# Optimization experiments

Measured on AMD Instinct MI355X. Metric: run time of the kernel, lower is better.

The kernel has to match this reference:

```python
import jax, jax.numpy as jnp
import numpy as np

DILATED = (1, 2, 3)
NUM_PROTOS = 100
PROTO_SIZE = 4
ENC_SIZE = 1600
NUM_CLASSES = 2
B, L = 64, 256

# num_filters split exactly as in torch: floor(P/len) each, first gets remainder
_nf = [NUM_PROTOS // len(DILATED)] * len(DILATED)
_nf[0] += NUM_PROTOS % len(DILATED)
NUM_FILTERS = tuple(_nf)  # (34, 33, 33)


def setup_inputs() -> dict:
    key = jax.random.key(0)
    k1, k2, k3 = jax.random.split(key, 3)
    embedding = jax.random.normal(k1, (B, L, ENC_SIZE), dtype=jnp.float32)
    # nn.init.uniform_ default is U[0,1)
    protolayer = jax.random.uniform(k2, (NUM_PROTOS, ENC_SIZE, PROTO_SIZE), dtype=jnp.float32)
    fc_w = jax.random.normal(k3, (NUM_CLASSES, NUM_PROTOS), dtype=jnp.float32) * 0.1
    return {"embedding": embedding, "protolayer": protolayer, "fc_w": fc_w}


def _l2_convolution(x_bel, protolayer):
    # x_bel: [B, L, E] -> [B, E, L] for NCH conv layout
    x = jnp.transpose(x_bel, (0, 2, 1))
    # sliding-window sum of x^2 computed ONCE per dilation (shared across protos,
    # mathematically identical to conv1d with all-ones weight)
    s = jnp.sum(x * x, axis=1)  # [B, L]
    p2_sum = jnp.sum(protolayer * protolayer, axis=(1, 2))  # [P]
    distances = []
    j = 0
    Lx = x.shape[2]
    for d, n in zip(DILATED, NUM_FILTERS):
        L_out = Lx - (PROTO_SIZE - 1) * d
        # windowed sum over K=PROTO_SIZE taps with dilation d: [B, L_out]
        x2_patch = sum(s[:, k * d:k * d + L_out] for k in range(PROTO_SIZE))
        # dilated cross-correlation x * p : [B, n, L_out]
        xp = jax.lax.conv_general_dilated(
            x, protolayer[j:j + n],
            window_strides=(1,), padding='VALID', rhs_dilation=(d,),
            dimension_numbers=('NCH', 'OIH', 'NCH'))
        dist = jnp.sqrt(jnp.abs(x2_patch[:, None, :] - 2.0 * xp
                                + p2_sum[j:j + n][None, :, None]))
        distances.append(dist)
        j += n
    return distances


def reference(embedding, protolayer, fc_w):
    distances = _l2_convolution(embedding, protolayer)
    prototype_distances = jnp.concatenate(
        [jnp.min(d, axis=2) for d in distances], axis=1)  # [B, P]
    class_out = prototype_distances @ fc_w.T  # [B, num_classes]
    return (prototype_distances, distances[0], distances[1], distances[2], class_out)
```

## Files before the change

kernel.cpp:

```cpp
#include <hip/hip_runtime.h>

#define B_   64
#define L_   256
#define E_   1600
#define P_   100
#define KP   4
#define N0 34
#define N1 33
#define N2 33
#define LOUT0 253
#define LOUT1 250
#define LOUT2 247
#define OFF_PD 0
#define OFF_D0 6400
#define OFF_D1 (OFF_D0 + B_*N0*LOUT0)
#define OFF_D2 (OFF_D1 + B_*N1*LOUT1)
#define OFF_CO (OFF_D2 + B_*N2*LOUT2)

#define WS_BT   0ull
#define WS_P2   1280000ull
#define WS_NEED (WS_P2 + 512ull)

#define TM2   144
#define BOFF4 36864

typedef float f32x4 __attribute__((ext_vector_type(4)));
typedef float f32x8 __attribute__((ext_vector_type(8)));
typedef unsigned short ushort8v __attribute__((ext_vector_type(8)));
typedef __bf16 bf16x8 __attribute__((ext_vector_type(8)));
typedef _Float16 f16;

__device__ __forceinline__ unsigned short bf16rne(float f) {
    unsigned u = __float_as_uint(f);
    u += 0x7FFFu + ((u >> 16) & 1u);
    return (unsigned short)(u >> 16);
}

typedef __attribute__((address_space(3))) void lds_void_t;
typedef __attribute__((address_space(1))) void glb_void_t;

__device__ __forceinline__ void gload16(const void* g, void* l) {
    __builtin_amdgcn_global_load_lds((const glb_void_t*)g, (lds_void_t*)l, 16, 0, 0);
}


__global__ __launch_bounds__(256) void proto_prepB_fast(
        const float* __restrict__ proto, char* __restrict__ ws,
        float* __restrict__ out) {
    int q = blockIdx.x;
    int wave = threadIdx.x >> 6, lane = threadIdx.x & 63;
    if (q < 25) {
        int p = q * 4 + wave;
        const float4* r = (const float4*)(proto + (size_t)p * (E_ * KP));
        unsigned short* bt = (unsigned short*)(ws + WS_BT);
        float acc = 0.f;
        #pragma unroll
        for (int it = 0; it < 25; ++it) {
            int e = it * 64 + lane;
            float4 v = r[e];
            acc += v.x*v.x + v.y*v.y + v.z*v.z + v.w*v.w;
            bt[(size_t)(4*p + 0) * E_ + e] = bf16rne(v.x);
            bt[(size_t)(4*p + 1) * E_ + e] = bf16rne(v.y);
            bt[(size_t)(4*p + 2) * E_ + e] = bf16rne(v.z);
            bt[(size_t)(4*p + 3) * E_ + e] = bf16rne(v.w);
        }
        #pragma unroll
        for (int off = 32; off; off >>= 1) acc += __shfl_down(acc, off);
        if (lane == 0) ((float*)(ws + WS_P2))[p] = acc;
    } else {
        for (int i = threadIdx.x; i < B_ * P_; i += 256)
            out[OFF_PD + i] = __uint_as_float(0x7F800000u);
    }
}

__global__ __launch_bounds__(192, 4) void proto_main_f32(
        const float* __restrict__ emb, const char* __restrict__ ws,
        float* __restrict__ out) {

    __shared__ __align__(16) char smem[47104];

    int bx    = blockIdx.x;
    int lb    = (bx & 7) * 80 + (bx >> 3);
    int b     = lb / 10;
    int inner = lb % 10;
    int m     = inner / 5;
    int n_blk = inner % 5;
    int r0    = m ? 112 : 0;
    int pbase = n_blk * 20;

    const char* Ag = (const char*)(emb + (size_t)(b * L_ + r0) * E_);
    const char* Bg = ws + WS_BT + (size_t)(pbase * 4) * 3200;

    int tid  = threadIdx.x;
    int lane = tid & 63;
    int wave = tid >> 6;
    int mrow = lane & 15;
    int jq   = lane >> 4;
    int a_lr = lane >> 4;
    int a_sl = lane & 15;
    int b_lr = lane >> 3;
    int b_sl = lane & 7;

    f32x4 acc[3][5] = {};
    float sacc[3] = {0.f, 0.f, 0.f};

    for (int c = 0; c < 25; ++c) {
        const char* Ac = Ag + c * 256;
        const char* Bc = Bg + c * 128;

        for (int t = wave; t < 10; t += 3) {
            int row = t * 8 + b_lr;
            gload16(Bc + (size_t)row * 3200 + ((b_sl ^ (row & 7)) * 16),
                    smem + BOFF4 + t * 1024);
        }
        for (int t = wave; t < 36; t += 3) {
            int row = t * 4 + a_lr;
            gload16(Ac + (size_t)row * 6400 + ((a_sl ^ (row & 15)) * 16),
                    smem + t * 1024);
        }
        __syncthreads();

        #pragma unroll
        for (int ks = 0; ks < 2; ++ks) {
            ushort8v af[3];
            #pragma unroll
            for (int mi = 0; mi < 3; ++mi) {
                int r  = wave * 48 + mi * 16 + mrow;
                int s0 = ks * 8 + jq * 2;
                f32x4 f0 = *(const f32x4*)(smem + r * 256 + ((s0 ^ (r & 15)) * 16));
                f32x4 f1 = *(const f32x4*)(smem + r * 256 + (((s0 + 1) ^ (r & 15)) * 16));
                sacc[mi] += f0[0]*f0[0] + f0[1]*f0[1] + f0[2]*f0[2] + f0[3]*f0[3]
                          + f1[0]*f1[0] + f1[1]*f1[1] + f1[2]*f1[2] + f1[3]*f1[3];
                f32x8 fv;
                fv[0]=f0[0]; fv[1]=f0[1]; fv[2]=f0[2]; fv[3]=f0[3];
                fv[4]=f1[0]; fv[5]=f1[1]; fv[6]=f1[2]; fv[7]=f1[3];
                af[mi] = __builtin_bit_cast(ushort8v,
                            __builtin_convertvector(fv, bf16x8));
            }
            ushort8v bfv[5];
            #pragma unroll
            for (int ni = 0; ni < 5; ++ni) {
                int rowB = ni * 16 + mrow;
                bfv[ni] = *(const ushort8v*)(smem + BOFF4 + rowB * 128
                            + (((ks << 2) + jq) ^ (rowB & 7)) * 16);
            }
            #pragma unroll
            for (int mi = 0; mi < 3; ++mi)
                #pragma unroll
                for (int ni = 0; ni < 5; ++ni)
                    acc[mi][ni] = __builtin_amdgcn_mfma_f32_16x16x32_bf16(
                        __builtin_bit_cast(bf16x8, af[mi]),
                        __builtin_bit_cast(bf16x8, bfv[ni]),
                        acc[mi][ni], 0, 0, 0);
        }
        __syncthreads();
    }

    f16*      Yh     = (f16*)smem;
    float*    slds   = (float*)(smem + 23328);
    float*    p2lds  = (float*)(smem + 23328 + 576);
    unsigned* minlds = (unsigned*)(smem + 23328 + 656);

    {
        int colq = lane & 15;
        int rowq = (lane >> 4) * 4;
        #pragma unroll
        for (int mi = 0; mi < 3; ++mi) {
            int row = wave * 48 + mi * 16 + rowq;
            #pragma unroll
            for (int ni = 0; ni < 5; ++ni) {
                int col = ni * 16 + colq;
                #pragma unroll
                for (int r = 0; r < 4; ++r)
                    Yh[(row + r) * 81 + col] = (f16)acc[mi][ni][r];
            }
        }
    }
    #pragma unroll
    for (int mi = 0; mi < 3; ++mi) {
        float v = sacc[mi];
        v += __shfl_xor(v, 16);
        v += __shfl_xor(v, 32);
        sacc[mi] = v;
    }
    if (jq == 0) {
        #pragma unroll
        for (int mi = 0; mi < 3; ++mi)
            slds[wave * 48 + mi * 16 + mrow] = sacc[mi];
    }
    if (tid < 20) {
        p2lds[tid] = ((const float*)(ws + WS_P2))[pbase + tid];
        minlds[tid] = 0x7F800000u;
    }
    __syncthreads();

    int l_lo = m * 128;
    for (int idx = tid; idx < 20 * 128; idx += 192) {
        int pl  = idx >> 7;
        int lof = idx & 127;
        int p = pbase + pl;
        int d, Lout, nseg, pseg; size_t segbase;
        if (p < 34)      { d = 1; Lout = LOUT0; segbase = OFF_D0; pseg = p;      nseg = N0; }
        else if (p < 67) { d = 2; Lout = LOUT1; segbase = OFF_D1; pseg = p - 34; nseg = N1; }
        else             { d = 3; Lout = LOUT2; segbase = OFF_D2; pseg = p - 67; nseg = N2; }
        int l = l_lo + lof;
        if (l < Lout) {
            int rl = l - r0;
            int c0 = pl * 4;
            float xp = (float)Yh[rl * 81 + c0]
                     + (float)Yh[(rl + d) * 81 + c0 + 1]
                     + (float)Yh[(rl + 2*d) * 81 + c0 + 2]
                     + (float)Yh[(rl + 3*d) * 81 + c0 + 3];
            float x2 = slds[rl] + slds[rl + d] + slds[rl + 2*d] + slds[rl + 3*d];
            float dist = sqrtf(fabsf(x2 - 2.f * xp + p2lds[pl]));
            out[segbase + ((size_t)b * nseg + pseg) * Lout + l] = dist;
            atomicMin(&minlds[pl], __float_as_uint(dist));
        }
    }
    __syncthreads();
    if (tid < 20)
        atomicMin((unsigned*)out + OFF_PD + b * P_ + pbase + tid, minlds[tid]);
}

#define TM   144
#define ASTR 40
#define YSTR 81

__global__ __launch_bounds__(256) void proto_prep_kernel(
        const float* __restrict__ emb, const float* __restrict__ proto,
        float* __restrict__ ws_s, float* __restrict__ ws_p2,
        float* __restrict__ out) {
    int q = blockIdx.x;
    int wave = threadIdx.x >> 6, lane = threadIdx.x & 63;
    if (q < 4096) {
        int row = q * 4 + wave;
        const float4* r = (const float4*)(emb + (size_t)row * E_);
        float acc = 0.f;
        #pragma unroll
        for (int it = 0; it < 7; ++it) {
            int e4 = it * 64 + lane;
            if (e4 < 400) {
                float4 v = r[e4];
                acc += v.x*v.x + v.y*v.y + v.z*v.z + v.w*v.w;
            }
        }
        #pragma unroll
        for (int off = 32; off; off >>= 1) acc += __shfl_down(acc, off);
        if (lane == 0) ws_s[row] = acc;
    } else if (q < 4121) {
        int p = (q - 4096) * 4 + wave;
        if (p < P_) {
            const float4* r = (const float4*)(proto + (size_t)p * (E_ * KP));
            float acc = 0.f;
            #pragma unroll
            for (int it = 0; it < 25; ++it) {
                float4 v = r[it * 64 + lane];
                acc += v.x*v.x + v.y*v.y + v.z*v.z + v.w*v.w;
            }
            #pragma unroll
            for (int off = 32; off; off >>= 1) acc += __shfl_down(acc, off);
            if (lane == 0) ws_p2[p] = acc;
        }
    } else {
        for (int i = threadIdx.x; i < B_ * P_; i += 256)
            out[OFF_PD + i] = __uint_as_float(0x7F800000u);
    }
}

__global__ __launch_bounds__(192) void proto_main_kernel(
        const float* __restrict__ emb, const float* __restrict__ proto,
        const float* __restrict__ ws_s, const float* __restrict__ ws_p2,
        float* __restrict__ out) {

    __shared__ __align__(16) char smem[47392];
    unsigned short* Ald = (unsigned short*)smem;
    unsigned short* Bld = (unsigned short*)(smem + TM*ASTR*2);

    int bx = blockIdx.x;
    int n_blk = bx % 5;
    int m     = (bx / 5) & 1;
    int b     = bx / 10;
    int r0    = m ? 112 : 0;
    int pbase = n_blk * 20;

    const float* Abase = emb + ((size_t)(b * L_ + r0)) * E_;
    const float* Bbase = proto + (size_t)pbase * (E_ * KP);

    int tid  = threadIdx.x;
    int lane = tid & 63;
    int wave = tid >> 6;
    int mrow = lane & 15;
    int kq   = (lane >> 4) * 8;

    f32x4 acc[3][5] = {};

    for (int c = 0; c < E_ / 32; ++c) {
        int e0 = c * 32;
        #pragma unroll
        for (int i = 0; i < 6; ++i) {
            int idx = tid + i * 192;
            int row = idx >> 3;
            int e4  = idx & 7;
            float4 v = *(const float4*)(Abase + (size_t)row * E_ + e0 + e4 * 4);
            ushort4 bv = make_ushort4(bf16rne(v.x), bf16rne(v.y),
                                      bf16rne(v.z), bf16rne(v.w));
            *(ushort4*)&Ald[row * ASTR + e4 * 4] = bv;
        }
        for (int idx = tid; idx < 640; idx += 192) {
            int pl = idx >> 5;
            int el = idx & 31;
            float4 v = *(const float4*)(Bbase + (size_t)pl * (E_ * KP)
                                        + (size_t)(e0 + el) * KP);
            Bld[(4*pl + 0) * ASTR + el] = bf16rne(v.x);
            Bld[(4*pl + 1) * ASTR + el] = bf16rne(v.y);
            Bld[(4*pl + 2) * ASTR + el] = bf16rne(v.z);
            Bld[(4*pl + 3) * ASTR + el] = bf16rne(v.w);
        }
        __syncthreads();

        ushort8v af[3], bfr[5];
        #pragma unroll
        for (int mi = 0; mi < 3; ++mi)
            af[mi] = *(const ushort8v*)&Ald[(wave*48 + mi*16 + mrow) * ASTR + kq];
        #pragma unroll
        for (int ni = 0; ni < 5; ++ni)
            bfr[ni] = *(const ushort8v*)&Bld[(ni*16 + mrow) * ASTR + kq];
        #pragma unroll
        for (int mi = 0; mi < 3; ++mi)
            #pragma unroll
            for (int ni = 0; ni < 5; ++ni)
                acc[mi][ni] = __builtin_amdgcn_mfma_f32_16x16x32_bf16(
                    __builtin_bit_cast(bf16x8, af[mi]),
                    __builtin_bit_cast(bf16x8, bfr[ni]),
                    acc[mi][ni], 0, 0, 0);
        __syncthreads();
    }

    float*    Ylds   = (float*)smem;
    float*    slds   = (float*)(smem + TM * YSTR * 4);
    float*    p2lds  = slds + TM;
    unsigned* minlds = (unsigned*)(p2lds + 20);

    {
        int colq = lane & 15;
        int rowq = (lane >> 4) * 4;
        #pragma unroll
        for (int mi = 0; mi < 3; ++mi) {
            int row = wave * 48 + mi * 16 + rowq;
            #pragma unroll
            for (int ni = 0; ni < 5; ++ni) {
                int col = ni * 16 + colq;
                #pragma unroll
                for (int r = 0; r < 4; ++r)
                    Ylds[(row + r) * YSTR + col] = acc[mi][ni][r];
            }
        }
    }
    if (tid < TM) slds[tid] = ws_s[b * L_ + r0 + tid];
    if (tid < 20) { p2lds[tid] = ws_p2[pbase + tid]; minlds[tid] = 0x7F800000u; }
    __syncthreads();

    int l_lo = m * 128;
    for (int idx = tid; idx < 20 * 128; idx += 192) {
        int pl  = idx >> 7;
        int lof = idx & 127;
        int p = pbase + pl;
        int d, Lout, nseg, pseg; size_t segbase;
        if (p < 34)      { d = 1; Lout = LOUT0; segbase = OFF_D0; pseg = p;      nseg = N0; }
        else if (p < 67) { d = 2; Lout = LOUT1; segbase = OFF_D1; pseg = p - 34; nseg = N1; }
        else             { d = 3; Lout = LOUT2; segbase = OFF_D2; pseg = p - 67; nseg = N2; }
        int l = l_lo + lof;
        if (l < Lout) {
            int rl = l - r0;
            int c0 = pl * 4;
            float xp = Ylds[rl * YSTR + c0]
                     + Ylds[(rl + d) * YSTR + c0 + 1]
                     + Ylds[(rl + 2*d) * YSTR + c0 + 2]
                     + Ylds[(rl + 3*d) * YSTR + c0 + 3];
            float x2 = slds[rl] + slds[rl + d] + slds[rl + 2*d] + slds[rl + 3*d];
            float dist = sqrtf(fabsf(x2 - 2.f * xp + p2lds[pl]));
            out[segbase + ((size_t)b * nseg + pseg) * Lout + l] = dist;
            atomicMin(&minlds[pl], __float_as_uint(dist));
        }
    }
    __syncthreads();
    if (tid < 20)
        atomicMin((unsigned*)out + OFF_PD + b * P_ + pbase + tid, minlds[tid]);
}

__global__ __launch_bounds__(128) void proto_fc_kernel(
        const float* __restrict__ fc_w, float* __restrict__ out) {
    int t = threadIdx.x;
    int b = t >> 1, c = t & 1;
    const float* pd = out + OFF_PD + b * P_;
    const float* w  = fc_w + c * P_;
    float s = 0.f;
    #pragma unroll 4
    for (int p = 0; p < P_; ++p) s += pd[p] * w[p];
    out[OFF_CO + b * 2 + c] = s;
}

extern "C" void kernel_launch(void* const* d_in, const int* in_sizes, int n_in,
                              void* d_out, int out_size, void* d_ws, size_t ws_size,
                              hipStream_t stream) {
    const float* emb   = (const float*)d_in[0];
    const float* proto = (const float*)d_in[1];
    const float* fc_w  = (const float*)d_in[2];
    float* out  = (float*)d_out;

    if (ws_size >= WS_NEED) {
        char* ws = (char*)d_ws;
        proto_prepB_fast<<<26, 256, 0, stream>>>(proto, ws, out);
        proto_main_f32<<<640, 192, 0, stream>>>(emb, ws, out);
    } else {
        float* ws_s  = (float*)d_ws;
        float* ws_p2 = ws_s + B_ * L_;
        proto_prep_kernel<<<4122, 256, 0, stream>>>(emb, proto, ws_s, ws_p2, out);
        proto_main_kernel<<<640, 192, 0, stream>>>(emb, proto, ws_s, ws_p2, out);
    }
    proto_fc_kernel<<<1, 128, 0, stream>>>(fc_w, out);
}
```

Baseline: 215.8 us.

## Load GEMM operands directly from global into registers, pre-permute B fragments

The main GEMM loop no longer stages A (embedding) and B (bf16 prototypes) tiles through LDS with global_load_lds and barriers. Each lane now reads its MFMA fragments straight from global memory. The prep kernel writes the prototype matrix in a fragment-permuted layout, so each lane's B read is one contiguous 16-byte load. This removes LDS staging traffic and the per-chunk __syncthreads, and shrinks LDS use. In exchange, the A loads are strided 32-byte reads per lane with no software pipelining, the occupancy hint drops from 4 to 2, and latency hiding relies on having many waves in flight.

```diff
diff --git a/kernel.cpp b/kernel.cpp
--- a/kernel.cpp
+++ b/kernel.cpp
@@ -18,11 +18,8 @@
 #define OFF_CO (OFF_D2 + B_*N2*LOUT2)
 
 #define WS_BT   0ull
-#define WS_P2   1280000ull
+#define WS_P2   1310720ull
 #define WS_NEED (WS_P2 + 512ull)
-
-#define TM2   144
-#define BOFF4 36864
 
 typedef float f32x4 __attribute__((ext_vector_type(4)));
 typedef float f32x8 __attribute__((ext_vector_type(8)));
@@ -36,15 +33,8 @@
     return (unsigned short)(u >> 16);
 }
 
-typedef __attribute__((address_space(3))) void lds_void_t;
-typedef __attribute__((address_space(1))) void glb_void_t;
-
-__device__ __forceinline__ void gload16(const void* g, void* l) {
-    __builtin_amdgcn_global_load_lds((const glb_void_t*)g, (lds_void_t*)l, 16, 0, 0);
-}
-
-
-__global__ __launch_bounds__(256) void proto_prepB_fast(
+
+__global__ __launch_bounds__(256) void proto_prepB_perm(
         const float* __restrict__ proto, char* __restrict__ ws,
         float* __restrict__ out) {
     int q = blockIdx.x;
@@ -53,16 +43,24 @@
         int p = q * 4 + wave;
         const float4* r = (const float4*)(proto + (size_t)p * (E_ * KP));
         unsigned short* bt = (unsigned short*)(ws + WS_BT);
+        int nrt = p >> 2;
+        int mr0 = (p & 3) * 4;
         float acc = 0.f;
         #pragma unroll
         for (int it = 0; it < 25; ++it) {
             int e = it * 64 + lane;
             float4 v = r[e];
             acc += v.x*v.x + v.y*v.y + v.z*v.z + v.w*v.w;
-            bt[(size_t)(4*p + 0) * E_ + e] = bf16rne(v.x);
-            bt[(size_t)(4*p + 1) * E_ + e] = bf16rne(v.y);
-            bt[(size_t)(4*p + 2) * E_ + e] = bf16rne(v.z);
-            bt[(size_t)(4*p + 3) * E_ + e] = bf16rne(v.w);
+            int c  = e >> 6;
+            int ks = (e >> 5) & 1;
+            int jq = (e >> 3) & 3;
+            int j  = e & 7;
+            unsigned base = ((unsigned)((nrt * 25 + c) * 2 + ks) << 9)
+                          + (unsigned)((jq * 16 + mr0) * 8 + j);
+            bt[base]      = bf16rne(v.x);
+            bt[base + 8]  = bf16rne(v.y);
+            bt[base + 16] = bf16rne(v.z);
+            bt[base + 24] = bf16rne(v.w);
         }
         #pragma unroll
         for (int off = 32; off; off >>= 1) acc += __shfl_down(acc, off);
@@ -73,11 +71,11 @@
     }
 }
 
-__global__ __launch_bounds__(192, 4) void proto_main_f32(
+__global__ __launch_bounds__(192, 2) void proto_main_direct(
         const float* __restrict__ emb, const char* __restrict__ ws,
         float* __restrict__ out) {
 
-    __shared__ __align__(16) char smem[47104];
+    __shared__ __align__(16) char smem[24064];
 
     int bx    = blockIdx.x;
     int lb    = (bx & 7) * 80 + (bx >> 3);
@@ -88,61 +86,55 @@
     int r0    = m ? 112 : 0;
     int pbase = n_blk * 20;
 
-    const char* Ag = (const char*)(emb + (size_t)(b * L_ + r0) * E_);
-    const char* Bg = ws + WS_BT + (size_t)(pbase * 4) * 3200;
-
     int tid  = threadIdx.x;
     int lane = tid & 63;
     int wave = tid >> 6;
     int mrow = lane & 15;
     int jq   = lane >> 4;
-    int a_lr = lane >> 4;
-    int a_sl = lane & 15;
-    int b_lr = lane >> 3;
-    int b_sl = lane & 7;
+
+    const float* Aptr[3];
+    #pragma unroll
+    for (int mi = 0; mi < 3; ++mi) {
+        int row = b * L_ + r0 + wave * 48 + mi * 16 + mrow;
+        Aptr[mi] = emb + (size_t)row * E_ + jq * 8;
+    }
+    const char* Bptr[5];
+    #pragma unroll
+    for (int ni = 0; ni < 5; ++ni) {
+        int nrt = n_blk * 5 + ni;
+        Bptr[ni] = ws + WS_BT + (size_t)(nrt * 50) * 1024 + lane * 16;
+    }
 
     f32x4 acc[3][5] = {};
     float sacc[3] = {0.f, 0.f, 0.f};
 
     for (int c = 0; c < 25; ++c) {
-        const char* Ac = Ag + c * 256;
-        const char* Bc = Bg + c * 128;
-
-        for (int t = wave; t < 10; t += 3) {
-            int row = t * 8 + b_lr;
-            gload16(Bc + (size_t)row * 3200 + ((b_sl ^ (row & 7)) * 16),
-                    smem + BOFF4 + t * 1024);
-        }
-        for (int t = wave; t < 36; t += 3) {
-            int row = t * 4 + a_lr;
-            gload16(Ac + (size_t)row * 6400 + ((a_sl ^ (row & 15)) * 16),
-                    smem + t * 1024);
-        }
-        __syncthreads();
-
         #pragma unroll
         for (int ks = 0; ks < 2; ++ks) {
+            int k0   = c * 64 + ks * 32;
+            int boff = (c * 2 + ks) * 1024;
+            f32x4 f0[3], f1[3];
+            ushort8v bfv[5];
+            #pragma unroll
+            for (int mi = 0; mi < 3; ++mi) {
+                f0[mi] = *(const f32x4*)(Aptr[mi] + k0);
+                f1[mi] = *(const f32x4*)(Aptr[mi] + k0 + 4);
+            }
+            #pragma unroll
+            for (int ni = 0; ni < 5; ++ni)
+                bfv[ni] = *(const ushort8v*)(Bptr[ni] + boff);
             ushort8v af[3];
             #pragma unroll
             for (int mi = 0; mi < 3; ++mi) {
-                int r  = wave * 48 + mi * 16 + mrow;
-                int s0 = ks * 8 + jq * 2;
-                f32x4 f0 = *(const f32x4*)(smem + r * 256 + ((s0 ^ (r & 15)) * 16));
-                f32x4 f1 = *(const f32x4*)(smem + r * 256 + (((s0 + 1) ^ (r & 15)) * 16));
-                sacc[mi] += f0[0]*f0[0] + f0[1]*f0[1] + f0[2]*f0[2] + f0[3]*f0[3]
-                          + f1[0]*f1[0] + f1[1]*f1[1] + f1[2]*f1[2] + f1[3]*f1[3];
+                sacc[mi] += f0[mi][0]*f0[mi][0] + f0[mi][1]*f0[mi][1]
+                          + f0[mi][2]*f0[mi][2] + f0[mi][3]*f0[mi][3]
+                          + f1[mi][0]*f1[mi][0] + f1[mi][1]*f1[mi][1]
+                          + f1[mi][2]*f1[mi][2] + f1[mi][3]*f1[mi][3];
                 f32x8 fv;
-                fv[0]=f0[0]; fv[1]=f0[1]; fv[2]=f0[2]; fv[3]=f0[3];
-                fv[4]=f1[0]; fv[5]=f1[1]; fv[6]=f1[2]; fv[7]=f1[3];
+                fv[0]=f0[mi][0]; fv[1]=f0[mi][1]; fv[2]=f0[mi][2]; fv[3]=f0[mi][3];
+                fv[4]=f1[mi][0]; fv[5]=f1[mi][1]; fv[6]=f1[mi][2]; fv[7]=f1[mi][3];
                 af[mi] = __builtin_bit_cast(ushort8v,
                             __builtin_convertvector(fv, bf16x8));
-            }
-            ushort8v bfv[5];
-            #pragma unroll
-            for (int ni = 0; ni < 5; ++ni) {
-                int rowB = ni * 16 + mrow;
-                bfv[ni] = *(const ushort8v*)(smem + BOFF4 + rowB * 128
-                            + (((ks << 2) + jq) ^ (rowB & 7)) * 16);
             }
             #pragma unroll
             for (int mi = 0; mi < 3; ++mi)
@@ -153,13 +145,12 @@
                         __builtin_bit_cast(bf16x8, bfv[ni]),
                         acc[mi][ni], 0, 0, 0);
         }
-        __syncthreads();
     }
 
     f16*      Yh     = (f16*)smem;
     float*    slds   = (float*)(smem + 23328);
-    float*    p2lds  = (float*)(smem + 23328 + 576);
-    unsigned* minlds = (unsigned*)(smem + 23328 + 656);
+    float*    p2lds  = (float*)(smem + 23904);
+    unsigned* minlds = (unsigned*)(smem + 23984);
 
     {
         int colq = lane & 15;
@@ -410,8 +401,8 @@
 
     if (ws_size >= WS_NEED) {
         char* ws = (char*)d_ws;
-        proto_prepB_fast<<<26, 256, 0, stream>>>(proto, ws, out);
-        proto_main_f32<<<640, 192, 0, stream>>>(emb, ws, out);
+        proto_prepB_perm<<<26, 256, 0, stream>>>(proto, ws, out);
+        proto_main_direct<<<640, 192, 0, stream>>>(emb, ws, out);
     } else {
         float* ws_s  = (float*)d_ws;
         float* ws_p2 = ws_s + B_ * L_;
```

Result: slower. 272.6 us (+26.3%).
